# Performance work log

Hardware: AMD Instinct MI355X
Metric: run time of the kernel (lower is better)

The kernel has to match this reference:

```python
import jax, jax.numpy as jnp
import numpy as np

L, H, NH, V, T, B, K = 12, 768, 12, 30522, 512, 4, 21
DH = H // NH
INV_SQRT_DH = 1.0 / float(np.sqrt(DH))
NEG = -1e4  # BERT additive mask value
LN_EPS = 1e-12


def _ln(x, g, b):
    m = x.mean(-1, keepdims=True)
    v = jnp.var(x, axis=-1, keepdims=True)
    return (x - m) * jax.lax.rsqrt(v + LN_EPS) * g + b


def _encoder(input_ids, attention_mask, word_emb, pos_emb, tok_emb, emb_g, emb_b,
             Wqkv, bqkv, Wo, bo, ln1_g, ln1_b, W1, b1, W2, b2, ln2_g, ln2_b):
    Bv, Tv = input_ids.shape
    h = word_emb[input_ids] + pos_emb[None, :Tv] + tok_emb[0]  # token_type_ids = 0
    h = _ln(h, emb_g, emb_b)
    bias = (1.0 - attention_mask[:, None, None, :].astype(h.dtype)) * NEG  # [B,1,1,T]

    def layer(h, xs):
        wqkv, bq, wo, bo_, g1, b1_, w1, bb1, w2, bb2, g2, b2_ = xs
        qkv = h @ wqkv + bq  # [B,T,3H]
        q, k, v = jnp.split(qkv, 3, axis=-1)
        def hd(x):
            return x.reshape(Bv, Tv, NH, DH).transpose(0, 2, 1, 3)
        q, k, v = hd(q), hd(k), hd(v)
        scores = jnp.einsum('bhqd,bhkd->bhqk', q, k) * INV_SQRT_DH + bias
        ctx = jnp.einsum('bhqk,bhkd->bhqd', jax.nn.softmax(scores, axis=-1), v)
        ctx = ctx.transpose(0, 2, 1, 3).reshape(Bv, Tv, H)
        h = _ln(h + ctx @ wo + bo_, g1, b1_)  # post-LN (BERT)
        ff = jax.nn.gelu(h @ w1 + bb1, approximate=False) @ w2 + bb2
        h = _ln(h + ff, g2, b2_)
        return h, None

    h, _ = jax.lax.scan(layer, h, (Wqkv, bqkv, Wo, bo, ln1_g, ln1_b, W1, b1, W2, b2, ln2_g, ln2_b))
    return h


def _crf_nll(emissions, tags, mask, start, end, trans):
    # emissions [B,T,K], tags [B,T] int, mask [B,T] bool; torchcrf reduction='mean'
    Bv, Tv, Kv = emissions.shape
    maskf = mask.astype(emissions.dtype)
    # numerator: score of the gold path
    num = start[tags[:, 0]] + emissions[jnp.arange(Bv), 0, tags[:, 0]]
    em_t = jnp.take_along_axis(emissions, tags[..., None], axis=-1)[..., 0]  # [B,T]
    tr_t = trans[tags[:, :-1], tags[:, 1:]]  # [B,T-1]
    num = num + jnp.sum((tr_t + em_t[:, 1:]) * maskf[:, 1:], axis=1)
    last_idx = mask.sum(axis=1).astype(jnp.int32) - 1
    last_tag = jnp.take_along_axis(tags, last_idx[:, None], axis=1)[:, 0]
    num = num + end[last_tag]
    # denominator: forward algorithm (logsumexp recursion over time)
    alpha0 = start[None, :] + emissions[:, 0]  # [B,K]

    def step(alpha, xs):
        em, m = xs  # em [B,K], m [B] bool
        nxt = jax.scipy.special.logsumexp(alpha[:, :, None] + trans[None] + em[:, None, :], axis=1)
        return jnp.where(m[:, None], nxt, alpha), None

    alpha, _ = jax.lax.scan(step, alpha0, (emissions[:, 1:].transpose(1, 0, 2), mask[:, 1:].T))
    den = jax.scipy.special.logsumexp(alpha + end[None, :], axis=1)
    return -(num - den).mean()


def _viterbi(emissions, mask, start, end, trans):
    # Returns [B,T] int32 best paths; padded tail repeats the last valid tag.
    Bv, Tv, Kv = emissions.shape
    score0 = start[None, :] + emissions[:, 0]
    ident = jnp.broadcast_to(jnp.arange(Kv), (Bv, Kv))

    def step(score, xs):
        em, m = xs
        cand = score[:, :, None] + trans[None]  # [B,K_prev,K_next]
        idx = jnp.where(m[:, None], jnp.argmax(cand, axis=1), ident)
        nxt = jnp.max(cand, axis=1) + em
        return jnp.where(m[:, None], nxt, score), idx

    score, hist = jax.lax.scan(step, score0, (emissions[:, 1:].transpose(1, 0, 2), mask[:, 1:].T))
    last = jnp.argmax(score + end[None, :], axis=1)  # [B]

    def back(nxt_tag, idx):
        prev = jnp.take_along_axis(idx, nxt_tag[:, None], axis=1)[:, 0]
        return prev, nxt_tag

    tag0, rest = jax.lax.scan(back, last, hist, reverse=True)  # rest[i] = tag at t=i+1
    return jnp.concatenate([tag0[None], rest], axis=0).T.astype(jnp.int32)


def setup_inputs():
    key = jax.random.key(0)
    ks = jax.random.split(key, 16)
    s = 0.02

    def n(k, shape):
        return (s * jax.random.normal(k, shape)).astype(jnp.float32)

    def u(k, shape):
        return jax.random.uniform(k, shape, minval=-0.1, maxval=0.1).astype(jnp.float32)

    p = {}
    p['input_ids'] = jax.random.randint(ks[0], (B, T), 0, V)
    lengths = jax.random.randint(ks[1], (B,), T // 2, T + 1)
    p['attention_mask'] = (jnp.arange(T)[None, :] < lengths[:, None]).astype(jnp.int32)
    p['valid_mask'] = p['attention_mask']
    p['labels'] = jax.random.randint(ks[2], (B, T), 0, K)
    p['word_emb'] = n(ks[3], (V, H))
    p['pos_emb'] = n(ks[4], (T, H))
    p['tok_emb'] = n(ks[5], (2, H))
    p['emb_g'] = jnp.ones((H,), jnp.float32)
    p['emb_b'] = jnp.zeros((H,), jnp.float32)
    p['Wqkv'] = n(ks[6], (L, H, 3 * H))
    p['bqkv'] = jnp.zeros((L, 3 * H), jnp.float32)
    p['Wo'] = n(ks[7], (L, H, H))
    p['bo'] = jnp.zeros((L, H), jnp.float32)
    p['ln1_g'] = jnp.ones((L, H), jnp.float32)
    p['ln1_b'] = jnp.zeros((L, H), jnp.float32)
    p['W1'] = n(ks[8], (L, H, 4 * H))
    p['b1'] = jnp.zeros((L, 4 * H), jnp.float32)
    p['W2'] = n(ks[9], (L, 4 * H, H))
    p['b2'] = jnp.zeros((L, H), jnp.float32)
    p['ln2_g'] = jnp.ones((L, H), jnp.float32)
    p['ln2_b'] = jnp.zeros((L, H), jnp.float32)
    p['Wc'] = n(ks[10], (H, K))
    p['bc'] = jnp.zeros((K,), jnp.float32)
    p['crf_start'] = u(ks[11], (K,))
    p['crf_end'] = u(ks[12], (K,))
    p['crf_trans'] = u(ks[13], (K, K))
    return p


def reference(input_ids, attention_mask, valid_mask, labels,
              word_emb, pos_emb, tok_emb, emb_g, emb_b,
              Wqkv, bqkv, Wo, bo, ln1_g, ln1_b, W1, b1, W2, b2, ln2_g, ln2_b,
              Wc, bc, crf_start, crf_end, crf_trans):
    h = _encoder(input_ids, attention_mask, word_emb, pos_emb, tok_emb, emb_g, emb_b,
                 Wqkv, bqkv, Wo, bo, ln1_g, ln1_b, W1, b1, W2, b2, ln2_g, ln2_b)
    emissions = h @ Wc + bc  # dropout is identity in eval/reference mode
    mask = attention_mask.astype(bool)
    nll = _crf_nll(emissions, labels, mask, crf_start, crf_end, crf_trans)
    decoded = _viterbi(emissions, mask, crf_start, crf_end, crf_trans)
    return nll, decoded
```

## Files before the change

### kernel.cpp

```cpp
#include <hip/hip_runtime.h>
#include <math.h>

constexpr int NLAYER = 12;
constexpr int H = 768;
constexpr int NH = 12;
constexpr int DH = 64;
constexpr int T = 512;
constexpr int B = 4;
constexpr int K = 21;
constexpr int BT = B * T;
constexpr float NEGB = -10000.0f;
constexpr float LNEPS = 1e-12f;
constexpr float INV_SQRT_DH = 0.125f;

typedef __attribute__((ext_vector_type(8))) short bf16x8;
typedef __attribute__((ext_vector_type(4))) float f32x4;
typedef __attribute__((ext_vector_type(4))) unsigned short u16x4;

#define WAIT_VMCNT(n) asm volatile("s_waitcnt vmcnt(" #n ")")

__device__ __forceinline__ float wave_sum_f(float v) {
#pragma unroll
  for (int off = 32; off > 0; off >>= 1) v += __shfl_xor(v, off);
  return v;
}
__device__ __forceinline__ int wave_sum_i(int v) {
#pragma unroll
  for (int off = 32; off > 0; off >>= 1) v += __shfl_xor(v, off);
  return v;
}
__device__ __forceinline__ float readlane_f(float v, int i) {
  return __uint_as_float(__builtin_amdgcn_readlane(__float_as_uint(v), i));
}
__device__ __forceinline__ unsigned short f32_bf16_rn(float x) {
  unsigned int u = __float_as_uint(x);
  u += 0x7fffu + ((u >> 16) & 1u);
  return (unsigned short)(u >> 16);
}
__device__ __forceinline__ void split_bf16(float x, unsigned short& h, unsigned short& l) {
  h = f32_bf16_rn(x);
  float hf = __uint_as_float((unsigned int)h << 16);
  l = f32_bf16_rn(x - hf);
}
__device__ __forceinline__ void block_reduce_sum2(float& s, float& q) {
  __shared__ float red[8];
  s = wave_sum_f(s);
  q = wave_sum_f(q);
  int lane = threadIdx.x & 63, wid = threadIdx.x >> 6;
  if (lane == 0) { red[wid] = s; red[4 + wid] = q; }
  __syncthreads();
  s = red[0] + red[1] + red[2] + red[3];
  q = red[4] + red[5] + red[6] + red[7];
}

__global__ __launch_bounds__(256) void embed_ln_kernel(
    const int* __restrict__ ids, const float* __restrict__ wemb,
    const float* __restrict__ pemb, const float* __restrict__ temb,
    const float* __restrict__ g, const float* __restrict__ bta,
    float* __restrict__ h, unsigned short* __restrict__ hh,
    unsigned short* __restrict__ hl) {
  int row = blockIdx.x;
  int t = row % T;
  int id = ids[row];
  const float* wp = wemb + (size_t)id * H;
  const float* pp = pemb + (size_t)t * H;
  float x[3];
  float s = 0.f, q = 0.f;
#pragma unroll
  for (int i = 0; i < 3; i++) {
    int c = threadIdx.x + i * 256;
    x[i] = wp[c] + pp[c] + temb[c];
    s += x[i];
    q += x[i] * x[i];
  }
  block_reduce_sum2(s, q);
  float mean = s * (1.0f / H);
  float var = q * (1.0f / H) - mean * mean;
  float inv = rsqrtf(var + LNEPS);
#pragma unroll
  for (int i = 0; i < 3; i++) {
    int c = threadIdx.x + i * 256;
    float y = (x[i] - mean) * inv * g[c] + bta[c];
    h[(size_t)row * H + c] = y;
    unsigned short yh, yl;
    split_bf16(y, yh, yl);
    hh[(size_t)row * H + c] = yh;
    hl[(size_t)row * H + c] = yl;
  }
}

__global__ __launch_bounds__(256) void add_ln_kernel(
    float* __restrict__ h, const float* __restrict__ add,
    const float* __restrict__ g, const float* __restrict__ bta,
    unsigned short* __restrict__ hh, unsigned short* __restrict__ hl) {
  int row = blockIdx.x;
  size_t base = (size_t)row * H;
  float x[3];
  float s = 0.f, q = 0.f;
#pragma unroll
  for (int i = 0; i < 3; i++) {
    int c = threadIdx.x + i * 256;
    x[i] = h[base + c] + add[base + c];
    s += x[i];
    q += x[i] * x[i];
  }
  block_reduce_sum2(s, q);
  float mean = s * (1.0f / H);
  float var = q * (1.0f / H) - mean * mean;
  float inv = rsqrtf(var + LNEPS);
#pragma unroll
  for (int i = 0; i < 3; i++) {
    int c = threadIdx.x + i * 256;
    float y = (x[i] - mean) * inv * g[c] + bta[c];
    h[base + c] = y;
    unsigned short yh, yl;
    split_bf16(y, yh, yl);
    hh[base + c] = yh;
    hl[base + c] = yl;
  }
}

__global__ __launch_bounds__(256) void wconv_kernel(
    const float* __restrict__ w0, const float* __restrict__ w1,
    const float* __restrict__ w2, const float* __restrict__ w3,
    unsigned short* __restrict__ Wth, unsigned short* __restrict__ Wtl) {
  __shared__ float tile[32][33];
  int bid = blockIdx.x;
  const float* src;
  int Kd, N, tk, tn;
  size_t off;
  if (bid < 1728) {
    src = w0; Kd = 768; N = 2304; tk = bid / 72; tn = bid % 72; off = 0;
  } else if (bid < 2304) {
    int t2 = bid - 1728; src = w1; Kd = 768; N = 768; tk = t2 / 24; tn = t2 % 24;
    off = 1769472;
  } else if (bid < 4608) {
    int t2 = bid - 2304; src = w2; Kd = 768; N = 3072; tk = t2 / 96; tn = t2 % 96;
    off = 2359296;
  } else {
    int t2 = bid - 4608; src = w3; Kd = 3072; N = 768; tk = t2 / 24; tn = t2 % 24;
    off = 4718592;
  }
  int tid = threadIdx.x;
  int k0 = tk * 32, n0 = tn * 32;
  int r = tid >> 3, c = (tid & 7) * 4;
  float4 v = *(const float4*)(src + (size_t)(k0 + r) * N + n0 + c);
  tile[r][c + 0] = v.x; tile[r][c + 1] = v.y; tile[r][c + 2] = v.z; tile[r][c + 3] = v.w;
  __syncthreads();
  u16x4 hv, lv;
#pragma unroll
  for (int q2 = 0; q2 < 4; q2++) {
    unsigned short sh, sl;
    split_bf16(tile[c + q2][r], sh, sl);
    hv[q2] = sh; lv[q2] = sl;
  }
  size_t dst = off + (size_t)(n0 + r) * Kd + k0 + c;
  *(u16x4*)(Wth + dst) = hv;
  *(u16x4*)(Wtl + dst) = lv;
}

template <int BN, int OUTMODE>
__global__ __launch_bounds__(256) void gemm_bf3_kernel(
    const unsigned short* __restrict__ Ah, const unsigned short* __restrict__ Al,
    const unsigned short* __restrict__ Wth, const unsigned short* __restrict__ Wtl,
    const float* __restrict__ bias, float* __restrict__ C,
    unsigned short* __restrict__ Ch, unsigned short* __restrict__ Cl,
    unsigned short* __restrict__ Kh, unsigned short* __restrict__ Kl,
    unsigned short* __restrict__ Vth, unsigned short* __restrict__ Vtl,
    int N, int Kd) {
  constexpr int WN = BN / 2;
  constexpr int FN = WN / 16;
  constexpr int AW = 128 * 32;
  constexpr int WW = BN * 32;
  constexpr int DBS = 2 * AW + 2 * WW;
  __shared__ short lds_s[2 * DBS];
  int tid = threadIdx.x;
  int lane = tid & 63, wid = tid >> 6;
  int wr = wid >> 1, wc = wid & 1;
  int bm = blockIdx.y * 128, bn = blockIdx.x * BN;
  f32x4 acc[4][FN] = {};
  int lrow = lane >> 2;
  int lslot_sw = (lane & 3) ^ ((lrow >> 1) & 3);

  const unsigned short* sbase;
  int rowbase, ldsoff, nchunks;
  if (wid == 0)      { sbase = Ah;  rowbase = bm; ldsoff = 0;            nchunks = 8; }
  else if (wid == 1) { sbase = Al;  rowbase = bm; ldsoff = AW;           nchunks = 8; }
  else if (wid == 2) { sbase = Wth; rowbase = bn; ldsoff = 2 * AW;       nchunks = BN / 16; }
  else               { sbase = Wtl; rowbase = bn; ldsoff = 2 * AW + WW;  nchunks = BN / 16; }

  const unsigned short* srcbase = sbase + (size_t)(rowbase + lrow) * Kd + lslot_sw * 8;

  auto STAGE = [&](int db, int k0) {
#pragma unroll
    for (int c = 0; c < 8; c++) {
      if (c < nchunks) {
        const unsigned short* src = srcbase + (size_t)(c * 16) * Kd + k0;
        char* dst = ((char*)lds_s) + (db * DBS + ldsoff) * 2 + c * 1024 + lane * 16;
        __builtin_amdgcn_global_load_lds(
            (const __attribute__((address_space(1))) void*)src,
            (__attribute__((address_space(3))) void*)dst, 16, 0, 0);
      }
    }
  };

  const int NT = Kd / 32;
  STAGE(0, 0);
  for (int kt = 0; kt < NT; kt++) {
    int cur = kt & 1;
    bool more = (kt + 1 < NT);
    if (more) STAGE(cur ^ 1, (kt + 1) * 32);
    if (more) {
      if (BN == 128 || wid < 2) { WAIT_VMCNT(8); } else { WAIT_VMCNT(4); }
    } else {
      WAIT_VMCNT(0);
    }
    __builtin_amdgcn_s_barrier();
    __builtin_amdgcn_sched_barrier(0);

    int lr = lane & 15, lg = lane >> 4;
    int slot = (lg ^ ((lr >> 1) & 3)) * 8;
    int cb = cur * DBS;
    bf16x8 af_h[4], af_l[4], wf_h[FN], wf_l[FN];
#pragma unroll
    for (int i = 0; i < 4; i++) {
      int e = (wr * 64 + i * 16 + lr) * 32 + slot;
      af_h[i] = *(const bf16x8*)&lds_s[cb + e];
      af_l[i] = *(const bf16x8*)&lds_s[cb + AW + e];
    }
#pragma unroll
    for (int j = 0; j < FN; j++) {
      int e = (wc * WN + j * 16 + lr) * 32 + slot;
      wf_h[j] = *(const bf16x8*)&lds_s[cb + 2 * AW + e];
      wf_l[j] = *(const bf16x8*)&lds_s[cb + 2 * AW + WW + e];
    }
#pragma unroll
    for (int i = 0; i < 4; i++)
#pragma unroll
      for (int j = 0; j < FN; j++) {
        acc[i][j] = __builtin_amdgcn_mfma_f32_16x16x32_bf16(af_h[i], wf_h[j], acc[i][j], 0, 0, 0);
        acc[i][j] = __builtin_amdgcn_mfma_f32_16x16x32_bf16(af_l[i], wf_h[j], acc[i][j], 0, 0, 0);
        acc[i][j] = __builtin_amdgcn_mfma_f32_16x16x32_bf16(af_h[i], wf_l[j], acc[i][j], 0, 0, 0);
      }
    asm volatile("s_waitcnt lgkmcnt(0)");
    __builtin_amdgcn_sched_barrier(0);
    __builtin_amdgcn_s_barrier();
    __builtin_amdgcn_sched_barrier(0);
  }

  int lr = lane & 15, lg = lane >> 4;
#pragma unroll
  for (int i = 0; i < 4; i++) {
#pragma unroll
    for (int j = 0; j < FN; j++) {
      int row = bm + wr * 64 + i * 16 + lg * 4;
      int col = bn + wc * WN + j * 16 + lr;
      float bv = bias[col];
      if (OUTMODE == 2) {
        int sec = col / 768;
        int within = col % 768;
        int hidx = within >> 6, d = within & 63;
        int b = row >> 9, t = row & 511;
        int bh = b * NH + hidx;
        if (sec == 2) {
          u16x4 hv, lv;
#pragma unroll
          for (int r = 0; r < 4; r++) {
            unsigned short sh, sl;
            split_bf16(acc[i][j][r] + bv, sh, sl);
            hv[r] = sh; lv[r] = sl;
          }
          size_t idx = ((size_t)bh * 64 + d) * T + t;
          *(u16x4*)(Vth + idx) = hv;
          *(u16x4*)(Vtl + idx) = lv;
        } else {
          unsigned short* dh = (sec == 0) ? Ch : Kh;
          unsigned short* dl = (sec == 0) ? Cl : Kl;
#pragma unroll
          for (int r = 0; r < 4; r++) {
            unsigned short sh, sl;
            split_bf16(acc[i][j][r] + bv, sh, sl);
            size_t idx = ((size_t)bh * T + t + r) * 64 + d;
            dh[idx] = sh;
            dl[idx] = sl;
          }
        }
      } else {
#pragma unroll
        for (int r = 0; r < 4; r++) {
          float v = acc[i][j][r] + bv;
          if (OUTMODE == 1) {
            v = 0.5f * v * (1.0f + erff(v * 0.70710678118654752f));
            unsigned short sh, sl;
            split_bf16(v, sh, sl);
            Ch[(size_t)(row + r) * N + col] = sh;
            Cl[(size_t)(row + r) * N + col] = sl;
          } else {
            C[(size_t)(row + r) * N + col] = v;
          }
        }
      }
    }
  }
}

__global__ __launch_bounds__(256) void attn_kernel(
    const unsigned short* __restrict__ qh, const unsigned short* __restrict__ ql,
    const unsigned short* __restrict__ kh, const unsigned short* __restrict__ kl,
    const unsigned short* __restrict__ vth, const unsigned short* __restrict__ vtl,
    const int* __restrict__ mask,
    unsigned short* __restrict__ cth, unsigned short* __restrict__ ctl) {
  int bh = blockIdx.y;
  int b = bh / NH, hidx = bh % NH;
  int i0 = blockIdx.x * 64;
  int tid = threadIdx.x, lane = tid & 63, w = tid >> 6;
  int lr = lane & 15, lg = lane >> 4;
  __shared__ float bias_s[T];
  __shared__ short p_h[4][16 * 64];
  __shared__ short p_l[4][16 * 64];
  for (int i = tid; i < T; i += 256)
    bias_s[i] = (1.0f - (float)mask[b * T + i]) * NEGB;
  __syncthreads();

  const unsigned short* qb_h = qh + ((size_t)bh * T + i0 + w * 16 + lr) * 64 + lg * 8;
  const unsigned short* qb_l = ql + ((size_t)bh * T + i0 + w * 16 + lr) * 64 + lg * 8;
  bf16x8 qf_h0 = *(const bf16x8*)qb_h;
  bf16x8 qf_h1 = *(const bf16x8*)(qb_h + 32);
  bf16x8 qf_l0 = *(const bf16x8*)qb_l;
  bf16x8 qf_l1 = *(const bf16x8*)(qb_l + 32);

  float m_run[4], l_run[4];
#pragma unroll
  for (int r = 0; r < 4; r++) { m_run[r] = -3.0e38f; l_run[r] = 0.f; }
  f32x4 acc_o[4] = {};

  for (int kt = 0; kt < T / 64; kt++) {
    f32x4 s[4] = {};
#pragma unroll
    for (int jf = 0; jf < 4; jf++) {
      size_t kb = ((size_t)bh * T + kt * 64 + jf * 16 + lr) * 64 + lg * 8;
      bf16x8 kf_h0 = *(const bf16x8*)(kh + kb);
      bf16x8 kf_h1 = *(const bf16x8*)(kh + kb + 32);
      bf16x8 kf_l0 = *(const bf16x8*)(kl + kb);
      bf16x8 kf_l1 = *(const bf16x8*)(kl + kb + 32);
      s[jf] = __builtin_amdgcn_mfma_f32_16x16x32_bf16(qf_h0, kf_h0, s[jf], 0, 0, 0);
      s[jf] = __builtin_amdgcn_mfma_f32_16x16x32_bf16(qf_h1, kf_h1, s[jf], 0, 0, 0);
      s[jf] = __builtin_amdgcn_mfma_f32_16x16x32_bf16(qf_l0, kf_h0, s[jf], 0, 0, 0);
      s[jf] = __builtin_amdgcn_mfma_f32_16x16x32_bf16(qf_l1, kf_h1, s[jf], 0, 0, 0);
      s[jf] = __builtin_amdgcn_mfma_f32_16x16x32_bf16(qf_h0, kf_l0, s[jf], 0, 0, 0);
      s[jf] = __builtin_amdgcn_mfma_f32_16x16x32_bf16(qf_h1, kf_l1, s[jf], 0, 0, 0);
    }
    float mt[4] = {-3.0e38f, -3.0e38f, -3.0e38f, -3.0e38f};
#pragma unroll
    for (int jf = 0; jf < 4; jf++) {
      float bcol = bias_s[kt * 64 + jf * 16 + lr];
#pragma unroll
      for (int r = 0; r < 4; r++) {
        float v = s[jf][r] * INV_SQRT_DH + bcol;
        s[jf][r] = v;
        mt[r] = fmaxf(mt[r], v);
      }
    }
#pragma unroll
    for (int r = 0; r < 4; r++) {
      mt[r] = fmaxf(mt[r], __shfl_xor(mt[r], 1));
      mt[r] = fmaxf(mt[r], __shfl_xor(mt[r], 2));
      mt[r] = fmaxf(mt[r], __shfl_xor(mt[r], 4));
      mt[r] = fmaxf(mt[r], __shfl_xor(mt[r], 8));
    }
#pragma unroll
    for (int r = 0; r < 4; r++) {
      float mn = fmaxf(m_run[r], mt[r]);
      float sc = __expf(m_run[r] - mn);
      m_run[r] = mn;
      l_run[r] *= sc;
#pragma unroll
      for (int jf = 0; jf < 4; jf++) acc_o[jf][r] *= sc;
    }
    float ps[4] = {0.f, 0.f, 0.f, 0.f};
#pragma unroll
    for (int jf = 0; jf < 4; jf++) {
#pragma unroll
      for (int r = 0; r < 4; r++) {
        float p = __expf(s[jf][r] - m_run[r]);
        ps[r] += p;
        unsigned short sh, sl;
        split_bf16(p, sh, sl);
        int q = lg * 4 + r;
        int col = jf * 16 + lr;
        int addr = q * 64 + (((col >> 3) ^ (q & 7)) << 3) + (col & 7);
        p_h[w][addr] = sh;
        p_l[w][addr] = sl;
      }
    }
#pragma unroll
    for (int r = 0; r < 4; r++) {
      ps[r] += __shfl_xor(ps[r], 1);
      ps[r] += __shfl_xor(ps[r], 2);
      ps[r] += __shfl_xor(ps[r], 4);
      ps[r] += __shfl_xor(ps[r], 8);
      l_run[r] += ps[r];
    }
#pragma unroll
    for (int c = 0; c < 2; c++) {
      int aaddr = lr * 64 + (((4 * c + lg) ^ (lr & 7)) << 3);
      bf16x8 pa_h = *(const bf16x8*)&p_h[w][aaddr];
      bf16x8 pa_l = *(const bf16x8*)&p_l[w][aaddr];
#pragma unroll
      for (int jf = 0; jf < 4; jf++) {
        size_t vb = ((size_t)bh * 64 + jf * 16 + lr) * T + kt * 64 + c * 32 + lg * 8;
        bf16x8 vf_h = *(const bf16x8*)(vth + vb);
        bf16x8 vf_l = *(const bf16x8*)(vtl + vb);
        acc_o[jf] = __builtin_amdgcn_mfma_f32_16x16x32_bf16(pa_h, vf_h, acc_o[jf], 0, 0, 0);
        acc_o[jf] = __builtin_amdgcn_mfma_f32_16x16x32_bf16(pa_l, vf_h, acc_o[jf], 0, 0, 0);
        acc_o[jf] = __builtin_amdgcn_mfma_f32_16x16x32_bf16(pa_h, vf_l, acc_o[jf], 0, 0, 0);
      }
    }
  }
  float inv[4];
#pragma unroll
  for (int r = 0; r < 4; r++) inv[r] = 1.0f / l_run[r];
#pragma unroll
  for (int jf = 0; jf < 4; jf++) {
#pragma unroll
    for (int r = 0; r < 4; r++) {
      float v = acc_o[jf][r] * inv[r];
      unsigned short sh, sl;
      split_bf16(v, sh, sl);
      size_t idx = ((size_t)(b * T) + i0 + w * 16 + lg * 4 + r) * H + hidx * 64 + jf * 16 + lr;
      cth[idx] = sh;
      ctl[idx] = sl;
    }
  }
}

__global__ __launch_bounds__(256) void classifier_kernel(
    const float* __restrict__ h, const float* __restrict__ Wc,
    const float* __restrict__ bc, float* __restrict__ em) {
  int id = blockIdx.x * 256 + threadIdx.x;
  if (id >= BT * K) return;
  int row = id / K, k = id % K;
  float acc = bc[k];
  const float* hr = h + (size_t)row * H;
  for (int d = 0; d < H; d++) acc = fmaf(hr[d], Wc[d * K + k], acc);
  em[id] = acc;
}

#define MRG(vo, io, va, ia, vb, ib) \
  float vo = ((vb) > (va)) ? (vb) : (va); \
  int io = ((vb) > (va)) ? (ib) : (ia);

__global__ __launch_bounds__(64) void crf_fused_kernel(
    const float* __restrict__ em, const int* __restrict__ labels,
    const int* __restrict__ mask, const float* __restrict__ start,
    const float* __restrict__ endv, const float* __restrict__ trans,
    float* __restrict__ parts, float* __restrict__ outdec) {
  __shared__ float em_s[T * K];
  __shared__ int mask_s[T];
  __shared__ unsigned char hist_s[(T - 1) * K];
  __shared__ float sc_s[32];
  int b = blockIdx.x & 3;
  int role = blockIdx.x >> 2;
  int j = threadIdx.x;
  const float* eb = em + (size_t)b * T * K;
  for (int i = j; i < T * K / 4; i += 64)
    ((float4*)em_s)[i] = ((const float4*)eb)[i];
  for (int i = j; i < T; i += 64) mask_s[i] = mask[b * T + i];
  __syncthreads();
  bool act = (j < K);
  float tr[K];
#pragma unroll
  for (int i = 0; i < K; i++) tr[i] = act ? trans[i * K + j] : 0.f;

  int cntloc = 0;
  for (int t = j; t < T; t += 64) cntloc += mask_s[t];
  int cnt = wave_sum_i(cntloc);

  if (role == 0) {
    const int* tb = labels + b * T;
    float numloc = 0.f;
    for (int t = j; t < T; t += 64) {
      if (t >= 1 && mask_s[t]) {
        int tp = tb[t - 1], tc = tb[t];
        numloc += trans[tp * K + tc] + em_s[t * K + tc];
      }
    }
    float num = wave_sum_f(numloc);
    float etr[K];
#pragma unroll
    for (int i = 0; i < K; i++) etr[i] = __expf(tr[i]);
    float alpha = act ? (start[j] + em_s[j]) : 0.f;
    float emv = act ? em_s[K + j] : 0.f;
    for (int t = 1; t < cnt; t++) {
      float emv_n = (act && (t + 1) < cnt) ? em_s[(t + 1) * K + j] : 0.f;
      float m0 = readlane_f(alpha, 0);
      float ee = __expf(alpha - m0);
      float e0 = readlane_f(ee, 0),  e1 = readlane_f(ee, 1),  e2 = readlane_f(ee, 2);
      float e3 = readlane_f(ee, 3),  e4 = readlane_f(ee, 4),  e5 = readlane_f(ee, 5);
      float e6 = readlane_f(ee, 6),  e7 = readlane_f(ee, 7),  e8 = readlane_f(ee, 8);
      float e9 = readlane_f(ee, 9),  e10 = readlane_f(ee, 10), e11 = readlane_f(ee, 11);
      float e12 = readlane_f(ee, 12), e13 = readlane_f(ee, 13), e14 = readlane_f(ee, 14);
      float e15 = readlane_f(ee, 15), e16 = readlane_f(ee, 16), e17 = readlane_f(ee, 17);
      float e18 = readlane_f(ee, 18), e19 = readlane_f(ee, 19), e20 = readlane_f(ee, 20);
      float a0 = fmaf(e16, etr[16], fmaf(e12, etr[12], fmaf(e8, etr[8],  fmaf(e4, etr[4], e0 * etr[0]))));
      float a1 = fmaf(e17, etr[17], fmaf(e13, etr[13], fmaf(e9, etr[9],  fmaf(e5, etr[5], e1 * etr[1]))));
      float a2 = fmaf(e18, etr[18], fmaf(e14, etr[14], fmaf(e10, etr[10], fmaf(e6, etr[6], e2 * etr[2]))));
      float a3 = fmaf(e19, etr[19], fmaf(e15, etr[15], fmaf(e11, etr[11], fmaf(e7, etr[7], e3 * etr[3]))));
      float ssum = fmaf(e20, etr[20], (a0 + a1) + (a2 + a3));
      float nxt = __logf(ssum) + m0 + emv;
      if (act) alpha = nxt;
      emv = emv_n;
    }
    float aj = act ? (alpha + endv[j]) : -3.0e38f;
    float mm = aj;
#pragma unroll
    for (int off = 32; off > 0; off >>= 1) mm = fmaxf(mm, __shfl_xor(mm, off));
    float e2v = act ? __expf(aj - mm) : 0.f;
    float s2 = wave_sum_f(e2v);
    float den = __logf(s2) + mm;
    if (j == 0) {
      int tag0 = tb[0];
      float numtot = num + start[tag0] + em_s[tag0] + endv[tb[cnt - 1]];
      parts[b] = numtot - den;
    }
  } else {
    float score = act ? (start[j] + em_s[j]) : 0.f;
    float emv = act ? em_s[K + j] : 0.f;
    for (int t = 1; t < cnt; t++) {
      float emv_n = (act && (t + 1) < cnt) ? em_s[(t + 1) * K + j] : 0.f;
      float c0 = readlane_f(score, 0) + tr[0],   c1 = readlane_f(score, 1) + tr[1];
      float c2 = readlane_f(score, 2) + tr[2],   c3 = readlane_f(score, 3) + tr[3];
      float c4 = readlane_f(score, 4) + tr[4],   c5 = readlane_f(score, 5) + tr[5];
      float c6 = readlane_f(score, 6) + tr[6],   c7 = readlane_f(score, 7) + tr[7];
      float c8 = readlane_f(score, 8) + tr[8],   c9 = readlane_f(score, 9) + tr[9];
      float c10 = readlane_f(score, 10) + tr[10], c11 = readlane_f(score, 11) + tr[11];
      float c12 = readlane_f(score, 12) + tr[12], c13 = readlane_f(score, 13) + tr[13];
      float c14 = readlane_f(score, 14) + tr[14], c15 = readlane_f(score, 15) + tr[15];
      float c16 = readlane_f(score, 16) + tr[16], c17 = readlane_f(score, 17) + tr[17];
      float c18 = readlane_f(score, 18) + tr[18], c19 = readlane_f(score, 19) + tr[19];
      float c20 = readlane_f(score, 20) + tr[20];
      MRG(m0v, m0i, c0, 0, c1, 1)
      MRG(m1v, m1i, c2, 2, c3, 3)
      MRG(m2v, m2i, c4, 4, c5, 5)
      MRG(m3v, m3i, c6, 6, c7, 7)
      MRG(m4v, m4i, c8, 8, c9, 9)
      MRG(m5v, m5i, c10, 10, c11, 11)
      MRG(m6v, m6i, c12, 12, c13, 13)
      MRG(m7v, m7i, c14, 14, c15, 15)
      MRG(m8v, m8i, c16, 16, c17, 17)
      MRG(m9v, m9i, c18, 18, c19, 19)
      MRG(p0v, p0i, m0v, m0i, m1v, m1i)
      MRG(p1v, p1i, m2v, m2i, m3v, m3i)
      MRG(p2v, p2i, m4v, m4i, m5v, m5i)
      MRG(p3v, p3i, m6v, m6i, m7v, m7i)
      MRG(p4v, p4i, m8v, m8i, m9v, m9i)
      MRG(r0v, r0i, p0v, p0i, p1v, p1i)
      MRG(r1v, r1i, p2v, p2i, p3v, p3i)
      MRG(r2v, r2i, p4v, p4i, c20, 20)
      MRG(s0v, s0i, r0v, r0i, r1v, r1i)
      MRG(fv, fi, s0v, s0i, r2v, r2i)
      if (act) {
        hist_s[(t - 1) * K + j] = (unsigned char)fi;
        score = fv + emv;
      }
      emv = emv_n;
    }
    if (act) sc_s[j] = score + endv[j];
    __syncthreads();
    if (j == 0) {
      float best = -3.0e38f;
      int last = 0;
#pragma unroll
      for (int i = 0; i < K; i++)
        if (sc_s[i] > best) { best = sc_s[i]; last = i; }
      for (int t = cnt - 1; t < T; t++) outdec[b * T + t] = (float)last;
      int cur = last;
      for (int t = cnt - 1; t >= 1; t--) {
        cur = hist_s[(t - 1) * K + cur];
        outdec[b * T + (t - 1)] = (float)cur;
      }
    }
  }
}

__global__ void nll_final_kernel(const float* __restrict__ parts,
                                 float* __restrict__ out) {
  out[0] = -0.25f * (parts[0] + parts[1] + parts[2] + parts[3]);
}

extern "C" void kernel_launch(void* const* d_in, const int* in_sizes, int n_in,
                              void* d_out, int out_size, void* d_ws, size_t ws_size,
                              hipStream_t stream) {
  (void)in_sizes; (void)n_in; (void)out_size; (void)ws_size;
  const int* ids    = (const int*)d_in[0];
  const int* amask  = (const int*)d_in[1];
  const int* labels = (const int*)d_in[3];
  const float* wemb = (const float*)d_in[4];
  const float* pemb = (const float*)d_in[5];
  const float* temb = (const float*)d_in[6];
  const float* eg   = (const float*)d_in[7];
  const float* ebta = (const float*)d_in[8];
  const float* Wqkv = (const float*)d_in[9];
  const float* bqkv = (const float*)d_in[10];
  const float* Wo   = (const float*)d_in[11];
  const float* bo   = (const float*)d_in[12];
  const float* ln1g = (const float*)d_in[13];
  const float* ln1b = (const float*)d_in[14];
  const float* W1   = (const float*)d_in[15];
  const float* b1   = (const float*)d_in[16];
  const float* W2   = (const float*)d_in[17];
  const float* b2   = (const float*)d_in[18];
  const float* ln2g = (const float*)d_in[19];
  const float* ln2b = (const float*)d_in[20];
  const float* Wc   = (const float*)d_in[21];
  const float* bc   = (const float*)d_in[22];
  const float* cst  = (const float*)d_in[23];
  const float* cen  = (const float*)d_in[24];
  const float* ctr  = (const float*)d_in[25];
  float* out = (float*)d_out;

  float* ws = (float*)d_ws;
  float* fp = ws;
  float* h = fp;                 fp += 1572864;
  unsigned short* hh  = (unsigned short*)fp; fp += 786432;
  unsigned short* hl  = (unsigned short*)fp; fp += 786432;
  unsigned short* qhp = (unsigned short*)fp; fp += 786432;
  unsigned short* qlp = (unsigned short*)fp; fp += 786432;
  unsigned short* khp = (unsigned short*)fp; fp += 786432;
  unsigned short* klp = (unsigned short*)fp; fp += 786432;
  unsigned short* vtp = (unsigned short*)fp; fp += 786432;
  unsigned short* vlp = (unsigned short*)fp; fp += 786432;
  unsigned short* cth = (unsigned short*)fp; fp += 786432;
  unsigned short* ctl = (unsigned short*)fp; fp += 786432;
  float* tmp = fp;               fp += 1572864;
  unsigned short* gh  = (unsigned short*)fp; fp += 3145728;
  unsigned short* gl  = (unsigned short*)fp; fp += 3145728;
  unsigned short* Wth = (unsigned short*)fp; fp += 3538944;
  unsigned short* Wtl = (unsigned short*)fp; fp += 3538944;
  float* em = fp;                fp += 43008;
  float* parts = fp;

  embed_ln_kernel<<<BT, 256, 0, stream>>>(ids, wemb, pemb, temb, eg, ebta, h, hh, hl);

  for (int l = 0; l < NLAYER; l++) {
    const float* bqkv_l = bqkv + (size_t)l * 3 * H;
    const float* bo_l   = bo + (size_t)l * H;
    const float* b1_l   = b1 + (size_t)l * 4 * H;
    const float* b2_l   = b2 + (size_t)l * H;

    wconv_kernel<<<6912, 256, 0, stream>>>(
        Wqkv + (size_t)l * H * 3 * H, Wo + (size_t)l * H * H,
        W1 + (size_t)l * H * 4 * H, W2 + (size_t)l * 4 * H * H, Wth, Wtl);

    gemm_bf3_kernel<128, 2><<<dim3(18, 16), 256, 0, stream>>>(
        hh, hl, Wth, Wtl, bqkv_l, nullptr, qhp, qlp, khp, klp, vtp, vlp, 3 * H, H);
    attn_kernel<<<dim3(T / 64, B * NH), 256, 0, stream>>>(
        qhp, qlp, khp, klp, vtp, vlp, amask, cth, ctl);
    gemm_bf3_kernel<64, 0><<<dim3(12, 16), 256, 0, stream>>>(
        cth, ctl, Wth + 1769472, Wtl + 1769472, bo_l, tmp,
        nullptr, nullptr, nullptr, nullptr, nullptr, nullptr, H, H);
    add_ln_kernel<<<BT, 256, 0, stream>>>(h, tmp, ln1g + (size_t)l * H, ln1b + (size_t)l * H, hh, hl);
    gemm_bf3_kernel<128, 1><<<dim3(24, 16), 256, 0, stream>>>(
        hh, hl, Wth + 2359296, Wtl + 2359296, b1_l, nullptr, gh, gl,
        nullptr, nullptr, nullptr, nullptr, 4 * H, H);
    gemm_bf3_kernel<64, 0><<<dim3(12, 16), 256, 0, stream>>>(
        gh, gl, Wth + 4718592, Wtl + 4718592, b2_l, tmp,
        nullptr, nullptr, nullptr, nullptr, nullptr, nullptr, H, 4 * H);
    add_ln_kernel<<<BT, 256, 0, stream>>>(h, tmp, ln2g + (size_t)l * H, ln2b + (size_t)l * H, hh, hl);
  }

  classifier_kernel<<<(BT * K + 255) / 256, 256, 0, stream>>>(h, Wc, bc, em);
  crf_fused_kernel<<<8, 64, 0, stream>>>(em, labels, amask, cst, cen, ctr, parts, out + 1);
  nll_final_kernel<<<1, 1, 0, stream>>>(parts, out);
}
```

Measured before the change: 3.278 ms.

## Use 64x128 GEMM tiles with XCD-aware block remap and transposed classifier weights

Every bf16x3 GEMM now uses one 64x128 tile shape on a 1D grid. Block indices are remapped so that consecutive tiles land on the same XCD, which should improve L2 reuse and give more blocks for occupancy across the CUs. The classifier weight matrix is transposed once so the classifier kernel can use contiguous float4 loads. Smaller M tiles lower per-block reuse of the weight tiles, and the remap assumes the grid size is a multiple of 8.

```diff
diff --git a/kernel.cpp b/kernel.cpp
--- a/kernel.cpp
+++ b/kernel.cpp
@@ -159,7 +159,7 @@
   *(u16x4*)(Wtl + dst) = lv;
 }
 
-template <int BN, int OUTMODE>
+template <int OUTMODE>
 __global__ __launch_bounds__(256) void gemm_bf3_kernel(
     const unsigned short* __restrict__ Ah, const unsigned short* __restrict__ Al,
     const unsigned short* __restrict__ Wth, const unsigned short* __restrict__ Wtl,
@@ -167,27 +167,29 @@
     unsigned short* __restrict__ Ch, unsigned short* __restrict__ Cl,
     unsigned short* __restrict__ Kh, unsigned short* __restrict__ Kl,
     unsigned short* __restrict__ Vth, unsigned short* __restrict__ Vtl,
-    int N, int Kd) {
-  constexpr int WN = BN / 2;
-  constexpr int FN = WN / 16;
-  constexpr int AW = 128 * 32;
-  constexpr int WW = BN * 32;
+    int N, int Kd, int ncols) {
+  constexpr int AW = 64 * 32;
+  constexpr int WW = 128 * 32;
   constexpr int DBS = 2 * AW + 2 * WW;
   __shared__ short lds_s[2 * DBS];
   int tid = threadIdx.x;
   int lane = tid & 63, wid = tid >> 6;
   int wr = wid >> 1, wc = wid & 1;
-  int bm = blockIdx.y * 128, bn = blockIdx.x * BN;
-  f32x4 acc[4][FN] = {};
+  int tiles = gridDim.x;
+  int q8 = tiles >> 3;
+  int wg = (blockIdx.x & 7) * q8 + (blockIdx.x >> 3);
+  int bm = (wg / ncols) * 64, bn = (wg % ncols) * 128;
+
+  f32x4 acc[2][4] = {};
   int lrow = lane >> 2;
   int lslot_sw = (lane & 3) ^ ((lrow >> 1) & 3);
 
   const unsigned short* sbase;
   int rowbase, ldsoff, nchunks;
-  if (wid == 0)      { sbase = Ah;  rowbase = bm; ldsoff = 0;            nchunks = 8; }
-  else if (wid == 1) { sbase = Al;  rowbase = bm; ldsoff = AW;           nchunks = 8; }
-  else if (wid == 2) { sbase = Wth; rowbase = bn; ldsoff = 2 * AW;       nchunks = BN / 16; }
-  else               { sbase = Wtl; rowbase = bn; ldsoff = 2 * AW + WW;  nchunks = BN / 16; }
+  if (wid == 0)      { sbase = Ah;  rowbase = bm; ldsoff = 0;            nchunks = 4; }
+  else if (wid == 1) { sbase = Al;  rowbase = bm; ldsoff = AW;           nchunks = 4; }
+  else if (wid == 2) { sbase = Wth; rowbase = bn; ldsoff = 2 * AW;       nchunks = 8; }
+  else               { sbase = Wtl; rowbase = bn; ldsoff = 2 * AW + WW;  nchunks = 8; }
 
   const unsigned short* srcbase = sbase + (size_t)(rowbase + lrow) * Kd + lslot_sw * 8;
 
@@ -211,7 +213,7 @@
     bool more = (kt + 1 < NT);
     if (more) STAGE(cur ^ 1, (kt + 1) * 32);
     if (more) {
-      if (BN == 128 || wid < 2) { WAIT_VMCNT(8); } else { WAIT_VMCNT(4); }
+      if (wid < 2) { WAIT_VMCNT(4); } else { WAIT_VMCNT(8); }
     } else {
       WAIT_VMCNT(0);
     }
@@ -221,23 +223,23 @@
     int lr = lane & 15, lg = lane >> 4;
     int slot = (lg ^ ((lr >> 1) & 3)) * 8;
     int cb = cur * DBS;
-    bf16x8 af_h[4], af_l[4], wf_h[FN], wf_l[FN];
-#pragma unroll
-    for (int i = 0; i < 4; i++) {
-      int e = (wr * 64 + i * 16 + lr) * 32 + slot;
+    bf16x8 af_h[2], af_l[2], wf_h[4], wf_l[4];
+#pragma unroll
+    for (int i = 0; i < 2; i++) {
+      int e = (wr * 32 + i * 16 + lr) * 32 + slot;
       af_h[i] = *(const bf16x8*)&lds_s[cb + e];
       af_l[i] = *(const bf16x8*)&lds_s[cb + AW + e];
     }
 #pragma unroll
-    for (int j = 0; j < FN; j++) {
-      int e = (wc * WN + j * 16 + lr) * 32 + slot;
+    for (int j = 0; j < 4; j++) {
+      int e = (wc * 64 + j * 16 + lr) * 32 + slot;
       wf_h[j] = *(const bf16x8*)&lds_s[cb + 2 * AW + e];
       wf_l[j] = *(const bf16x8*)&lds_s[cb + 2 * AW + WW + e];
     }
 #pragma unroll
-    for (int i = 0; i < 4; i++)
-#pragma unroll
-      for (int j = 0; j < FN; j++) {
+    for (int i = 0; i < 2; i++)
+#pragma unroll
+      for (int j = 0; j < 4; j++) {
         acc[i][j] = __builtin_amdgcn_mfma_f32_16x16x32_bf16(af_h[i], wf_h[j], acc[i][j], 0, 0, 0);
         acc[i][j] = __builtin_amdgcn_mfma_f32_16x16x32_bf16(af_l[i], wf_h[j], acc[i][j], 0, 0, 0);
         acc[i][j] = __builtin_amdgcn_mfma_f32_16x16x32_bf16(af_h[i], wf_l[j], acc[i][j], 0, 0, 0);
@@ -250,11 +252,11 @@
 
   int lr = lane & 15, lg = lane >> 4;
 #pragma unroll
-  for (int i = 0; i < 4; i++) {
-#pragma unroll
-    for (int j = 0; j < FN; j++) {
-      int row = bm + wr * 64 + i * 16 + lg * 4;
-      int col = bn + wc * WN + j * 16 + lr;
+  for (int i = 0; i < 2; i++) {
+#pragma unroll
+    for (int j = 0; j < 4; j++) {
+      int row = bm + wr * 32 + i * 16 + lg * 4;
+      int col = bn + wc * 64 + j * 16 + lr;
       float bv = bias[col];
       if (OUTMODE == 2) {
         int sec = col / 768;
@@ -434,15 +436,29 @@
   }
 }
 
+__global__ __launch_bounds__(256) void wct_kernel(
+    const float* __restrict__ Wc, float* __restrict__ WcT) {
+  int id = blockIdx.x * 256 + threadIdx.x;
+  int k = id / H, d = id % H;
+  WcT[id] = Wc[d * K + k];
+}
+
 __global__ __launch_bounds__(256) void classifier_kernel(
-    const float* __restrict__ h, const float* __restrict__ Wc,
+    const float* __restrict__ h, const float* __restrict__ WcT,
     const float* __restrict__ bc, float* __restrict__ em) {
   int id = blockIdx.x * 256 + threadIdx.x;
   if (id >= BT * K) return;
   int row = id / K, k = id % K;
+  const float4* h4 = (const float4*)(h + (size_t)row * H);
+  const float4* w4 = (const float4*)(WcT + (size_t)k * H);
   float acc = bc[k];
-  const float* hr = h + (size_t)row * H;
-  for (int d = 0; d < H; d++) acc = fmaf(hr[d], Wc[d * K + k], acc);
+  for (int d = 0; d < H / 4; d++) {
+    float4 a = h4[d], b = w4[d];
+    acc = fmaf(a.x, b.x, acc);
+    acc = fmaf(a.y, b.y, acc);
+    acc = fmaf(a.z, b.z, acc);
+    acc = fmaf(a.w, b.w, acc);
+  }
   em[id] = acc;
 }
 
@@ -638,9 +654,11 @@
   unsigned short* Wth = (unsigned short*)fp; fp += 3538944;
   unsigned short* Wtl = (unsigned short*)fp; fp += 3538944;
   float* em = fp;                fp += 43008;
-  float* parts = fp;
+  float* parts = fp;             fp += 8;
+  float* WcT = fp;               fp += 16128;
 
   embed_ln_kernel<<<BT, 256, 0, stream>>>(ids, wemb, pemb, temb, eg, ebta, h, hh, hl);
+  wct_kernel<<<63, 256, 0, stream>>>(Wc, WcT);
 
   for (int l = 0; l < NLAYER; l++) {
     const float* bqkv_l = bqkv + (size_t)l * 3 * H;
@@ -652,24 +670,25 @@
         Wqkv + (size_t)l * H * 3 * H, Wo + (size_t)l * H * H,
         W1 + (size_t)l * H * 4 * H, W2 + (size_t)l * 4 * H * H, Wth, Wtl);
 
-    gemm_bf3_kernel<128, 2><<<dim3(18, 16), 256, 0, stream>>>(
-        hh, hl, Wth, Wtl, bqkv_l, nullptr, qhp, qlp, khp, klp, vtp, vlp, 3 * H, H);
+    gemm_bf3_kernel<2><<<576, 256, 0, stream>>>(
+        hh, hl, Wth, Wtl, bqkv_l, nullptr, qhp, qlp, khp, klp, vtp, vlp,
+        3 * H, H, 18);
     attn_kernel<<<dim3(T / 64, B * NH), 256, 0, stream>>>(
         qhp, qlp, khp, klp, vtp, vlp, amask, cth, ctl);
-    gemm_bf3_kernel<64, 0><<<dim3(12, 16), 256, 0, stream>>>(
+    gemm_bf3_kernel<0><<<192, 256, 0, stream>>>(
         cth, ctl, Wth + 1769472, Wtl + 1769472, bo_l, tmp,
-        nullptr, nullptr, nullptr, nullptr, nullptr, nullptr, H, H);
+        nullptr, nullptr, nullptr, nullptr, nullptr, nullptr, H, H, 6);
     add_ln_kernel<<<BT, 256, 0, stream>>>(h, tmp, ln1g + (size_t)l * H, ln1b + (size_t)l * H, hh, hl);
-    gemm_bf3_kernel<128, 1><<<dim3(24, 16), 256, 0, stream>>>(
+    gemm_bf3_kernel<1><<<768, 256, 0, stream>>>(
         hh, hl, Wth + 2359296, Wtl + 2359296, b1_l, nullptr, gh, gl,
-        nullptr, nullptr, nullptr, nullptr, 4 * H, H);
-    gemm_bf3_kernel<64, 0><<<dim3(12, 16), 256, 0, stream>>>(
+        nullptr, nullptr, nullptr, nullptr, 4 * H, H, 24);
+    gemm_bf3_kernel<0><<<192, 256, 0, stream>>>(
         gh, gl, Wth + 4718592, Wtl + 4718592, b2_l, tmp,
-        nullptr, nullptr, nullptr, nullptr, nullptr, nullptr, H, 4 * H);
+        nullptr, nullptr, nullptr, nullptr, nullptr, nullptr, H, 4 * H, 6);
     add_ln_kernel<<<BT, 256, 0, stream>>>(h, tmp, ln2g + (size_t)l * H, ln2b + (size_t)l * H, hh, hl);
   }
 
-  classifier_kernel<<<(BT * K + 255) / 256, 256, 0, stream>>>(h, Wc, bc, em);
+  classifier_kernel<<<(BT * K + 255) / 256, 256, 0, stream>>>(h, WcT, bc, em);
   crf_fused_kernel<<<8, 64, 0, stream>>>(em, labels, amask, cst, cen, ctr, parts, out + 1);
   nll_final_kernel<<<1, 1, 0, stream>>>(parts, out);
 }
```

Result: no change. 3.221 ms (-1.8%).
